# Optimization experiments

Measured on AMD Instinct MI355X. Metric: run time of the kernel, lower is better.

Reference implementation:

```python
import math
import jax, jax.numpy as jnp
import numpy as np

B, H, T, D = 1, 16, 2048, 64
DIM = H * D
WINDOW = 256  # sliding window size


def sliding_window_mask(seq_len, window):
    # token i attends to tokens max(0, i-window+1) .. i
    row = jnp.arange(seq_len)[:, None]
    col = jnp.arange(seq_len)[None, :]
    return (col <= row) & (col > row - window)


def setup_inputs() -> dict:
    key = jax.random.key(0)
    kq, kk, kv, kw = jax.random.split(key, 4)
    q = jax.random.normal(kq, (B, H, T, D), dtype=jnp.float32)
    k = jax.random.normal(kk, (B, H, T, D), dtype=jnp.float32)
    v = jax.random.normal(kv, (B, H, T, D), dtype=jnp.float32)
    W_proj = jax.random.normal(kw, (DIM, DIM), dtype=jnp.float32) * (1.0 / math.sqrt(DIM))
    return {"q": q, "k": k, "v": v, "W_proj": W_proj}


def reference(q, k, v, W_proj):
    b, h, t, d = q.shape
    scale = 1.0 / math.sqrt(d)
    mask = sliding_window_mask(t, WINDOW)  # (T, T) bool
    # scaled dot-product attention logits: (B, H, T, T)
    att = jnp.einsum("bhqd,bhkd->bhqk", q, k) * scale
    att = jnp.where(mask, att, jnp.finfo(att.dtype).min)
    att = jax.nn.softmax(att, axis=-1)
    y = jnp.einsum("bhqk,bhkd->bhqd", att, v)  # (B, H, T, D)
    y = y.transpose(0, 2, 1, 3).reshape(b, t, h * d)  # (B, T, dim)
    return y @ W_proj  # c_proj, no bias
```

## Files before the change

kernel.cpp:

```cpp
#include <hip/hip_runtime.h>

#define T_SEQ 2048
#define NH    16
#define HD    64
#define DIM   1024
#define WIN   256

typedef __attribute__((ext_vector_type(4))) float f32x4;
typedef __attribute__((ext_vector_type(8))) short s16x8;
typedef unsigned short u16;

static __device__ __forceinline__ u16 f2bf(float f) {
    unsigned u = __builtin_bit_cast(unsigned, f);
    u += 0x7fff + ((u >> 16) & 1);
    return (u16)(u >> 16);
}

static __device__ __forceinline__ int fV(int d) { return (d & 7) ^ ((d >> 3) & 7); }

static __device__ __forceinline__ void gload16(const void* g, void* l) {
    __builtin_amdgcn_global_load_lds(
        (const __attribute__((address_space(1))) unsigned int*)g,
        (__attribute__((address_space(3))) unsigned int*)l, 16, 0, 0);
}

__global__ __launch_bounds__(256) void conv_kernel(const float* __restrict__ W,
                                                   u16* __restrict__ Wt,
                                                   const float* __restrict__ kg,
                                                   u16* __restrict__ Kc,
                                                   const float* __restrict__ vg,
                                                   u16* __restrict__ Vt) {
    __shared__ float sT[64][69];
    const int bid = (int)blockIdx.x;
    const int t   = threadIdx.x;

    if (bid < 256) {
        const int k0 = (bid & 15) * 64;
        const int n0 = (bid >> 4) * 64;
#pragma unroll
        for (int i = 0; i < 4; ++i) {
            const int idx = i * 256 + t;
            const int kr = idx >> 4, c4 = (idx & 15) * 4;
            float4 v = *(const float4*)(W + (size_t)(k0 + kr) * DIM + n0 + c4);
            sT[kr][c4] = v.x; sT[kr][c4 + 1] = v.y; sT[kr][c4 + 2] = v.z; sT[kr][c4 + 3] = v.w;
        }
        __syncthreads();
#pragma unroll
        for (int i = 0; i < 2; ++i) {
            const int idx = i * 256 + t;
            const int nr = idx >> 3, ch = (idx & 7) * 8;
            s16x8 o;
#pragma unroll
            for (int e = 0; e < 8; ++e) o[e] = f2bf(sT[ch + e][nr]);
            *(s16x8*)(Wt + (size_t)(n0 + nr) * DIM + k0 + ch) = o;
        }
    } else if (bid < 768) {
        const int vt  = bid - 256;
        const int h   = vt >> 5;
        const int kt0 = (vt & 31) * 64;
        const float* src = vg + ((size_t)h * T_SEQ + kt0) * HD;
#pragma unroll
        for (int i = 0; i < 4; ++i) {
            const int idx = i * 256 + t;
            const int kr = idx >> 4, c4 = (idx & 15) * 4;
            float4 v = *(const float4*)(src + (size_t)kr * HD + c4);
            sT[kr][c4] = v.x; sT[kr][c4 + 1] = v.y; sT[kr][c4 + 2] = v.z; sT[kr][c4 + 3] = v.w;
        }
        __syncthreads();
#pragma unroll
        for (int i = 0; i < 2; ++i) {
            const int idx = i * 256 + t;
            const int nr = idx >> 3, ch = (idx & 7) * 8;
            s16x8 o;
#pragma unroll
            for (int e = 0; e < 8; ++e) o[e] = f2bf(sT[ch + e][nr]);
            *(s16x8*)(Vt + ((size_t)h * HD + nr) * T_SEQ + kt0 + ch) = o;
        }
    } else {
        const int kb = bid - 768;
        const float* src = kg + (size_t)kb * 8192;
        u16* dst = Kc + (size_t)kb * 8192;
#pragma unroll
        for (int i = 0; i < 4; ++i) {
            const int off = i * 2048 + t * 8;
            float4 a = *(const float4*)(src + off);
            float4 b = *(const float4*)(src + off + 4);
            s16x8 o;
            o[0] = f2bf(a.x); o[1] = f2bf(a.y); o[2] = f2bf(a.z); o[3] = f2bf(a.w);
            o[4] = f2bf(b.x); o[5] = f2bf(b.y); o[6] = f2bf(b.z); o[7] = f2bf(b.w);
            *(s16x8*)(dst + off) = o;
        }
    }
}

__global__ __launch_bounds__(256) void attn_kernel(const float* __restrict__ qg,
                                                   const u16* __restrict__ Kc,
                                                   const u16* __restrict__ Vt,
                                                   u16* __restrict__ y) {
    __shared__ __align__(16) char sK[2][8192];
    __shared__ __align__(16) char sV[2][8192];
    __shared__ __align__(16) char sP[4][2048];

    const int ab   = (int)blockIdx.x;
    const int swzb = (ab & 7) * 64 + (ab >> 3);
    const int t    = threadIdx.x;
    const int lane = t & 63;
    const int w    = t >> 6;
    const int q0   = (swzb & 31) * 64;
    const int h    = swzb >> 5;

    const u16* Kh = Kc + (size_t)h * T_SEQ * HD;
    const u16* Vh = Vt + (size_t)h * HD * T_SEQ;

    const int lr = lane & 15;
    const int lg = lane >> 4;

    s16x8 qf[2];
    {
        const float* qrow = qg + ((size_t)h * T_SEQ + q0 + w * 16 + lr) * HD + lg * 8;
#pragma unroll
        for (int s = 0; s < 2; ++s) {
            float4 a = *(const float4*)(qrow + 32 * s);
            float4 b = *(const float4*)(qrow + 32 * s + 4);
            s16x8 f;
            f[0] = f2bf(a.x); f[1] = f2bf(a.y); f[2] = f2bf(a.z); f[3] = f2bf(a.w);
            f[4] = f2bf(b.x); f[5] = f2bf(b.y); f[6] = f2bf(b.z); f[7] = f2bf(b.w);
            qf[s] = f;
        }
    }

    f32x4 o[4];
#pragma unroll
    for (int i = 0; i < 4; ++i) o[i] = (f32x4){0.f, 0.f, 0.f, 0.f};
    float lsum[4] = {0.f, 0.f, 0.f, 0.f};

    int lo = q0 - (WIN - 1);
    if (lo < 0) lo = 0;
    const int kc0 = lo & ~63;
    const int nc  = (q0 - kc0) / 64 + 1;

    const int sRow8 = lane >> 3;
    const int sCh   = lane & 7;

#define STAGE(buf, kc)                                                              \
    do {                                                                            \
        _Pragma("unroll") for (int j = 0; j < 2; ++j) {                             \
            const int s_  = j * 4 + w;                                              \
            const int row = s_ * 8 + sRow8;                                         \
            gload16(Kh + (size_t)((kc) + row) * HD + ((sCh ^ (row & 7)) << 3),      \
                    sK[buf] + s_ * 1024);                                           \
            gload16(Vh + (size_t)row * T_SEQ + (kc) + ((sCh ^ fV(row)) << 3),       \
                    sV[buf] + s_ * 1024);                                           \
        }                                                                           \
    } while (0)

    STAGE(0, kc0);

    for (int ic = 0; ic < nc; ++ic) {
        const int kc = kc0 + ic * 64;
        const int cb = ic & 1;
        if (ic + 1 < nc) {
            STAGE(cb ^ 1, kc + 64);
            asm volatile("s_waitcnt vmcnt(4)" ::: "memory");
        } else {
            asm volatile("s_waitcnt vmcnt(0)" ::: "memory");
        }
        __builtin_amdgcn_s_barrier();

        char* pw = sP[w];
#pragma unroll
        for (int kt = 0; kt < 4; ++kt) {
            const int krow = kt * 16 + lr;
            const int kswz = (krow & 7) << 4;
            s16x8 kf0 = *(const s16x8*)(sK[cb] + krow * 128 + ((lg * 16) ^ kswz));
            s16x8 kf1 = *(const s16x8*)(sK[cb] + krow * 128 + ((lg * 16 + 64) ^ kswz));
            f32x4 s = (f32x4){0.f, 0.f, 0.f, 0.f};
            s = __builtin_amdgcn_mfma_f32_16x16x32_bf16(qf[0], kf0, s, 0, 0, 0);
            s = __builtin_amdgcn_mfma_f32_16x16x32_bf16(qf[1], kf1, s, 0, 0, 0);
            const int key = kc + kt * 16 + lr;
#pragma unroll
            for (int r = 0; r < 4; ++r) {
                const int qrow = q0 + w * 16 + lg * 4 + r;
                float pv = 0.f;
                if (key <= qrow && key > qrow - WIN) pv = __expf(s[r] * 0.125f);
                lsum[r] += pv;
                const int prow = lg * 4 + r;
                *(u16*)(pw + prow * 128 + ((kt * 32 + lr * 2) ^ ((prow & 7) << 4))) = f2bf(pv);
            }
        }

        s16x8 pf0 = *(const s16x8*)(pw + lr * 128 + ((lg * 16) ^ ((lr & 7) << 4)));
        s16x8 pf1 = *(const s16x8*)(pw + lr * 128 + ((lg * 16 + 64) ^ ((lr & 7) << 4)));
#pragma unroll
        for (int td = 0; td < 4; ++td) {
            const int drow = td * 16 + lr;
            const int vswz = fV(drow) << 4;
            s16x8 vf0 = *(const s16x8*)(sV[cb] + drow * 128 + ((lg * 16) ^ vswz));
            s16x8 vf1 = *(const s16x8*)(sV[cb] + drow * 128 + ((lg * 16 + 64) ^ vswz));
            o[td] = __builtin_amdgcn_mfma_f32_16x16x32_bf16(pf0, vf0, o[td], 0, 0, 0);
            o[td] = __builtin_amdgcn_mfma_f32_16x16x32_bf16(pf1, vf1, o[td], 0, 0, 0);
        }
        __builtin_amdgcn_s_barrier();
    }
#undef STAGE

#pragma unroll
    for (int m = 1; m < 16; m <<= 1) {
#pragma unroll
        for (int r = 0; r < 4; ++r) lsum[r] += __shfl_xor(lsum[r], m, 64);
    }
    float rl[4];
#pragma unroll
    for (int r = 0; r < 4; ++r) rl[r] = 1.f / lsum[r];
#pragma unroll
    for (int td = 0; td < 4; ++td)
#pragma unroll
        for (int r = 0; r < 4; ++r)
            y[(size_t)(q0 + w * 16 + lg * 4 + r) * DIM + h * HD + td * 16 + lr] =
                f2bf(o[td][r] * rl[r]);
}

__global__ __launch_bounds__(256) void proj_kernel(const u16* __restrict__ A,
                                                   const u16* __restrict__ Bt,
                                                   float* __restrict__ out) {
    __shared__ __align__(16) char sA[3][128 * 128];
    __shared__ __align__(16) char sB[3][64 * 128];

    const int t    = threadIdx.x;
    const int lane = t & 63;
    const int w    = t >> 6;
    const int wr   = w >> 1, wc = w & 1;
    const int lr   = lane & 15, lg = lane >> 4;

    const int id   = (int)blockIdx.x;
    const int wgid = (id & 7) * 32 + (id >> 3);
    const int m0   = (wgid >> 4) * 128;
    const int n0   = (wgid & 15) * 64;

    f32x4 acc[4][2];
#pragma unroll
    for (int i = 0; i < 4; ++i)
#pragma unroll
        for (int j = 0; j < 2; ++j) acc[i][j] = (f32x4){0.f, 0.f, 0.f, 0.f};

    const int sRow = lane >> 3;
    const int sCh  = lane & 7;

#define STAGE(buf, k0)                                                                 \
    do {                                                                               \
        _Pragma("unroll") for (int p = 0; p < 4; ++p) {                                \
            const int pi  = p * 4 + w;                                                 \
            const int row = pi * 8 + sRow;                                             \
            gload16(A + (size_t)(m0 + row) * DIM + (k0) + ((sCh ^ (row & 7)) << 3),    \
                    sA[buf] + pi * 1024);                                              \
        }                                                                              \
        _Pragma("unroll") for (int p = 0; p < 2; ++p) {                                \
            const int pi  = p * 4 + w;                                                 \
            const int row = pi * 8 + sRow;                                             \
            gload16(Bt + (size_t)(n0 + row) * DIM + (k0) + ((sCh ^ (row & 7)) << 3),   \
                    sB[buf] + pi * 1024);                                              \
        }                                                                              \
    } while (0)

    STAGE(0, 0);
    STAGE(1, 64);

#pragma unroll
    for (int kt = 0; kt < DIM / 64; ++kt) {
        const int cur  = kt % 3;
        const int nxt  = (kt + 2) % 3;
        const int knxt = ((kt + 2) & 15) * 64;

        STAGE(nxt, knxt);
        asm volatile("s_waitcnt vmcnt(12)" ::: "memory");
        __builtin_amdgcn_s_barrier();

        s16x8 af[2][4], bfr[2][2];
#pragma unroll
        for (int kh = 0; kh < 2; ++kh) {
#pragma unroll
            for (int mi = 0; mi < 4; ++mi) {
                const int row = wr * 64 + mi * 16 + lr;
                const int cc  = kh * 4 + lg;
                af[kh][mi] = *(const s16x8*)(sA[cur] + row * 128 + ((cc ^ (row & 7)) << 4));
            }
#pragma unroll
            for (int ni = 0; ni < 2; ++ni) {
                const int row = wc * 32 + ni * 16 + lr;
                const int cc  = kh * 4 + lg;
                bfr[kh][ni] = *(const s16x8*)(sB[cur] + row * 128 + ((cc ^ (row & 7)) << 4));
            }
        }
        __builtin_amdgcn_s_setprio(1);
#pragma unroll
        for (int kh = 0; kh < 2; ++kh)
#pragma unroll
            for (int mi = 0; mi < 4; ++mi)
#pragma unroll
                for (int ni = 0; ni < 2; ++ni)
                    acc[mi][ni] = __builtin_amdgcn_mfma_f32_16x16x32_bf16(
                        af[kh][mi], bfr[kh][ni], acc[mi][ni], 0, 0, 0);
        __builtin_amdgcn_s_setprio(0);
        __builtin_amdgcn_s_barrier();
    }
#undef STAGE

    asm volatile("s_waitcnt vmcnt(0)" ::: "memory");

#pragma unroll
    for (int mi = 0; mi < 4; ++mi)
#pragma unroll
        for (int ni = 0; ni < 2; ++ni)
#pragma unroll
            for (int r = 0; r < 4; ++r)
                out[(size_t)(m0 + wr * 64 + mi * 16 + lg * 4 + r) * DIM +
                    n0 + wc * 32 + ni * 16 + lr] = acc[mi][ni][r];
}

extern "C" void kernel_launch(void* const* d_in, const int* in_sizes, int n_in,
                              void* d_out, int out_size, void* d_ws, size_t ws_size,
                              hipStream_t stream) {
    const float* q = (const float*)d_in[0];
    const float* k = (const float*)d_in[1];
    const float* v = (const float*)d_in[2];
    const float* W = (const float*)d_in[3];
    float* out = (float*)d_out;

    u16* y_bf = (u16*)d_ws;
    u16* Wt   = y_bf + (size_t)T_SEQ * DIM;
    u16* Kc   = Wt + (size_t)DIM * DIM;
    u16* Vt   = Kc + (size_t)NH * T_SEQ * HD;

    conv_kernel<<<1024, 256, 0, stream>>>(W, Wt, k, Kc, v, Vt);
    attn_kernel<<<512, 256, 0, stream>>>(q, Kc, Vt, y_bf);
    proj_kernel<<<256, 256, 0, stream>>>(y_bf, Wt, out);
}
```

Baseline: 38.32 us.

## Fold softmax scale into Q, use exp2, skip masks on full tiles, double-buffer proj

The attention kernel now multiplies Q by scale*log2(e) before converting to bf16 and uses the hardware exp2 instruction in place of __expf. Key chunks that lie entirely inside the sliding window take a branch with no per-element mask checks. The projection GEMM drops from a triple-buffered to a double-buffered LDS pipeline with a prefetch distance of one, which lowers LDS use and may allow more blocks per CU, but leaves less latency hiding. Pre-scaling Q before bf16 rounding slightly changes numerics.

```diff
diff --git a/kernel.cpp b/kernel.cpp
--- a/kernel.cpp
+++ b/kernel.cpp
@@ -14,6 +14,10 @@
     unsigned u = __builtin_bit_cast(unsigned, f);
     u += 0x7fff + ((u >> 16) & 1);
     return (u16)(u >> 16);
+}
+
+static __device__ __forceinline__ float exp2fast(float x) {
+    return __builtin_amdgcn_exp2f(x);
 }
 
 static __device__ __forceinline__ int fV(int d) { return (d & 7) ^ ((d >> 3) & 7); }
@@ -115,6 +119,7 @@
     const int lr = lane & 15;
     const int lg = lane >> 4;
 
+    const float SCL = 0.125f * 1.44269504088896f;
     s16x8 qf[2];
     {
         const float* qrow = qg + ((size_t)h * T_SEQ + q0 + w * 16 + lr) * HD + lg * 8;
@@ -123,8 +128,10 @@
             float4 a = *(const float4*)(qrow + 32 * s);
             float4 b = *(const float4*)(qrow + 32 * s + 4);
             s16x8 f;
-            f[0] = f2bf(a.x); f[1] = f2bf(a.y); f[2] = f2bf(a.z); f[3] = f2bf(a.w);
-            f[4] = f2bf(b.x); f[5] = f2bf(b.y); f[6] = f2bf(b.z); f[7] = f2bf(b.w);
+            f[0] = f2bf(a.x * SCL); f[1] = f2bf(a.y * SCL);
+            f[2] = f2bf(a.z * SCL); f[3] = f2bf(a.w * SCL);
+            f[4] = f2bf(b.x * SCL); f[5] = f2bf(b.y * SCL);
+            f[6] = f2bf(b.z * SCL); f[7] = f2bf(b.w * SCL);
             qf[s] = f;
         }
     }
@@ -167,6 +174,8 @@
         }
         __builtin_amdgcn_s_barrier();
 
+        const bool fullValid = (kc >= lo) && (kc + 63 <= q0);
+
         char* pw = sP[w];
 #pragma unroll
         for (int kt = 0; kt < 4; ++kt) {
@@ -178,14 +187,24 @@
             s = __builtin_amdgcn_mfma_f32_16x16x32_bf16(qf[0], kf0, s, 0, 0, 0);
             s = __builtin_amdgcn_mfma_f32_16x16x32_bf16(qf[1], kf1, s, 0, 0, 0);
             const int key = kc + kt * 16 + lr;
-#pragma unroll
-            for (int r = 0; r < 4; ++r) {
-                const int qrow = q0 + w * 16 + lg * 4 + r;
-                float pv = 0.f;
-                if (key <= qrow && key > qrow - WIN) pv = __expf(s[r] * 0.125f);
-                lsum[r] += pv;
-                const int prow = lg * 4 + r;
-                *(u16*)(pw + prow * 128 + ((kt * 32 + lr * 2) ^ ((prow & 7) << 4))) = f2bf(pv);
+            if (fullValid) {
+#pragma unroll
+                for (int r = 0; r < 4; ++r) {
+                    const float pv = exp2fast(s[r]);
+                    lsum[r] += pv;
+                    const int prow = lg * 4 + r;
+                    *(u16*)(pw + prow * 128 + ((kt * 32 + lr * 2) ^ ((prow & 7) << 4))) = f2bf(pv);
+                }
+            } else {
+#pragma unroll
+                for (int r = 0; r < 4; ++r) {
+                    const int qrow = q0 + w * 16 + lg * 4 + r;
+                    float pv = 0.f;
+                    if (key <= qrow && key > qrow - WIN) pv = exp2fast(s[r]);
+                    lsum[r] += pv;
+                    const int prow = lg * 4 + r;
+                    *(u16*)(pw + prow * 128 + ((kt * 32 + lr * 2) ^ ((prow & 7) << 4))) = f2bf(pv);
+                }
             }
         }
 
@@ -223,8 +242,8 @@
 __global__ __launch_bounds__(256) void proj_kernel(const u16* __restrict__ A,
                                                    const u16* __restrict__ Bt,
                                                    float* __restrict__ out) {
-    __shared__ __align__(16) char sA[3][128 * 128];
-    __shared__ __align__(16) char sB[3][64 * 128];
+    __shared__ __align__(16) char sA[2][128 * 128];
+    __shared__ __align__(16) char sB[2][64 * 128];
 
     const int t    = threadIdx.x;
     const int lane = t & 63;
@@ -263,16 +282,16 @@
     } while (0)
 
     STAGE(0, 0);
-    STAGE(1, 64);
 
 #pragma unroll
     for (int kt = 0; kt < DIM / 64; ++kt) {
-        const int cur  = kt % 3;
-        const int nxt  = (kt + 2) % 3;
-        const int knxt = ((kt + 2) & 15) * 64;
-
-        STAGE(nxt, knxt);
-        asm volatile("s_waitcnt vmcnt(12)" ::: "memory");
+        const int cur = kt & 1;
+        if (kt + 1 < DIM / 64) {
+            STAGE(cur ^ 1, (kt + 1) * 64);
+            asm volatile("s_waitcnt vmcnt(6)" ::: "memory");
+        } else {
+            asm volatile("s_waitcnt vmcnt(0)" ::: "memory");
+        }
         __builtin_amdgcn_s_barrier();
 
         s16x8 af[2][4], bfr[2][2];
@@ -304,8 +323,6 @@
         __builtin_amdgcn_s_barrier();
     }
 #undef STAGE
-
-    asm volatile("s_waitcnt vmcnt(0)" ::: "memory");
 
 #pragma unroll
     for (int mi = 0; mi < 4; ++mi)
```

Measured after the change: 37.52 us. -2.1%, faster.
